# Kernel tuning notes

Hardware: AMD Instinct MI355X
Metric: run time of the kernel (lower is better)

The kernel has to match this reference:

```python
import jax, jax.numpy as jnp
import numpy as np
from jax import lax

PADDING = 1  # from init_kwargs; must equal (k-1)//2 so the residual add is shape-valid


def _conv_single(x, w):
    # x: [C_in, H, W], w: [C_out, C_in, kH, kW] -> [C_out, H, W]
    y = lax.conv_general_dilated(
        x[None],  # [1, C_in, H, W]
        w,
        window_strides=(1, 1),
        padding=[(PADDING, PADDING), (PADDING, PADDING)],
        dimension_numbers=("NCHW", "OIHW", "NCHW"),
    )
    return y[0]


def setup_inputs() -> dict:
    key = jax.random.key(0)
    k1, k2 = jax.random.split(key)
    B, C, H, W, K = 16, 128, 64, 64, 3
    inp = jax.random.normal(k1, (B, C, H, W), dtype=jnp.float32)
    # per-sample dynamic weights, scaled so conv output is O(1)
    weight = jax.random.normal(k2, (B, C, C, K, K), dtype=jnp.float32) * (1.0 / np.sqrt(C * K * K))
    return {"input": inp, "weight": weight}


def reference(input, weight):
    # per-sample conv2d with a different kernel per batch element + residual add
    residual = jax.vmap(_conv_single)(input, weight)  # [B, C, H, W]
    return input + residual
```

## Files before the change

### kernel.cpp

```cpp
#include <hip/hip_runtime.h>
#include <hip/hip_bf16.h>


typedef _Float16 h8 __attribute__((ext_vector_type(8)));
typedef _Float16 h4 __attribute__((ext_vector_type(4)));
typedef float f32x16 __attribute__((ext_vector_type(16)));
typedef float f4 __attribute__((ext_vector_type(4)));

#define MFMA32 __builtin_amdgcn_mfma_f32_32x32x16_f16

__global__ __launch_bounds__(256) void w_prepass(const float* __restrict__ W,
                                                 _Float16* __restrict__ wp) {
    __shared__ float raw[8 * 1153];
    const int bid = blockIdx.x;
    const int b   = bid >> 4;
    const int co0 = (bid & 15) * 8;
    const int t   = threadIdx.x;

    const float* src = W + (size_t)(b * 128 + co0) * 1152;
#pragma unroll
    for (int i = 0; i < 9; ++i) {
        int idx  = (i * 256 + t) * 4;
        f4 v     = *(const f4*)(src + idx);
        int co_l = idx / 1152;
        int rem  = idx - co_l * 1152;
        *(f4*)&raw[co_l * 1153 + rem] = v;
    }
    __syncthreads();

#pragma unroll
    for (int i = 0; i < 9; ++i) {
        int c    = i * 256 + t;
        int jh   = c & 1;
        int co_l = (c >> 1) & 7;
        int oct  = (c >> 4) & 3;
        int r    = c >> 6;
        int kw   = r % 3;
        int r2   = r / 3;
        int kc   = r2 & 3;
        int kh   = r2 >> 2;
        int cib  = kc * 32 + oct * 8 + jh * 4;
        h4 v;
#pragma unroll
        for (int jj = 0; jj < 4; ++jj)
            v[jj] = (_Float16)raw[co_l * 1153 + (cib + jj) * 9 + kh * 3 + kw];
        size_t o = ((size_t)(b * 3 + kh) * 4 + kc) * 12288 +
                   (size_t)(kw * 4 + oct) * 1024 + (size_t)(co0 + co_l) * 8 + jh * 4;
        *(h4*)&wp[o] = v;
    }
}


__global__ __launch_bounds__(256, 2) void conv_main(const float* __restrict__ X,
                                                    const _Float16* __restrict__ wp,
                                                    float* __restrict__ out) {
    __shared__ _Float16 sX[2 * 4 * 66 * 8];
    __shared__ _Float16 sW[12 * 128 * 8];

    const int t    = threadIdx.x;
    const int lane = t & 63;
    const int l31  = lane & 31;
    const int lhi  = lane >> 5;
    const int wv   = t >> 6;
    const int wvM  = wv >> 1;
    const int wr   = wv & 1;

    const int bid   = blockIdx.x;
    const int batch = bid >> 5;
    const int h0    = (bid & 31) * 2;

    const int sy  = t >> 7;
    const int xq  = (t & 15) * 4;
    const int cio = (t >> 4) & 7;

    f32x16 acc[2][2];
#pragma unroll
    for (int mt = 0; mt < 2; ++mt)
#pragma unroll
        for (int nt = 0; nt < 2; ++nt)
#pragma unroll
            for (int r = 0; r < 16; ++r) acc[mt][nt][r] = 0.f;

    if (t < 16) {
        int y = t >> 3, oct = (t >> 1) & 3, xp = (t & 1) * 65;
        h8 z;
#pragma unroll
        for (int j = 0; j < 8; ++j) z[j] = (_Float16)0.f;
        *(h8*)&sX[((y * 4 + oct) * 66 + xp) * 8] = z;
    }

    f4 xrv[4];
    h8 wreg[6];

    auto load_stage = [&](int s) {
        const int kh = s >> 2, kc = s & 3;
        const int yy = h0 + sy + kh - 1;
        if (yy >= 0 && yy < 64) {
            const float* xp = X + ((size_t)(batch * 128 + kc * 32 + cio * 4) * 64 + yy) * 64 + xq;
#pragma unroll
            for (int j = 0; j < 4; ++j) xrv[j] = *(const f4*)(xp + (size_t)j * 4096);
        } else {
#pragma unroll
            for (int j = 0; j < 4; ++j) xrv[j] = (f4){0.f, 0.f, 0.f, 0.f};
        }
        const _Float16* wsrc = wp + ((size_t)(batch * 3 + kh) * 4 + kc) * 12288 + t * 8;
#pragma unroll
        for (int r = 0; r < 6; ++r) wreg[r] = *(const h8*)(wsrc + (size_t)r * 2048);
    };
    auto write_stage = [&]() {
#pragma unroll
        for (int k = 0; k < 4; ++k) {
            h4 v = {(_Float16)xrv[0][k], (_Float16)xrv[1][k],
                    (_Float16)xrv[2][k], (_Float16)xrv[3][k]};
            *(h4*)&sX[((sy * 4 + (cio >> 1)) * 66 + xq + 1 + k) * 8 + (cio & 1) * 4] = v;
        }
#pragma unroll
        for (int r = 0; r < 6; ++r) *(h8*)&sW[(r * 256 + t) * 8] = wreg[r];
    };

    load_stage(0);
    __syncthreads();
    write_stage();
    __syncthreads();

#pragma unroll 1
    for (int s = 0; s < 12; ++s) {
        if (s < 11) load_stage(s + 1);

#pragma unroll
        for (int ks = 0; ks < 6; ++ks) {
            const int kw = ks >> 1, kk = ks & 1;
            h8 af[2], bf[2];
#pragma unroll
            for (int mt = 0; mt < 2; ++mt)
                af[mt] = *(const h8*)&sW[((kw * 4 + kk * 2 + lhi) * 128 + wvM * 64 + mt * 32 + l31) * 8];
#pragma unroll
            for (int nt = 0; nt < 2; ++nt)
                bf[nt] = *(const h8*)&sX[((wr * 4 + kk * 2 + lhi) * 66 + nt * 32 + l31 + kw) * 8];
#pragma unroll
            for (int mt = 0; mt < 2; ++mt)
#pragma unroll
                for (int nt = 0; nt < 2; ++nt)
                    acc[mt][nt] = MFMA32(af[mt], bf[nt], acc[mt][nt], 0, 0, 0);
        }

        if (s < 11) {
            __syncthreads();
            write_stage();
            __syncthreads();
        }
    }

#pragma unroll
    for (int mt = 0; mt < 2; ++mt)
#pragma unroll
        for (int nt = 0; nt < 2; ++nt)
#pragma unroll
            for (int rg = 0; rg < 16; ++rg) {
                int co = wvM * 64 + mt * 32 + (rg & 3) + 8 * (rg >> 2) + 4 * lhi;
                int x  = nt * 32 + l31;
                size_t o = ((size_t)(batch * 128 + co) * 64 + h0 + wr) * 64 + x;
                out[o] = X[o] + acc[mt][nt][rg];
            }
}

extern "C" void kernel_launch(void* const* d_in, const int* in_sizes, int n_in,
                              void* d_out, int out_size, void* d_ws, size_t ws_size,
                              hipStream_t stream) {
    const float* inp = (const float*)d_in[0];
    const float* wgt = (const float*)d_in[1];
    float* out = (float*)d_out;
    _Float16* wpk = (_Float16*)d_ws;

    w_prepass<<<256, 256, 0, stream>>>(wgt, wpk);
    conv_main<<<512, 256, 0, stream>>>(inp, wpk, out);
}
```

Before: 113.5 us.

## Double-buffer LDS and load weights directly to LDS via global_load_lds

Converts the single-buffered stage loop into a double-buffered pipeline with one barrier per stage instead of two. Weight tiles go straight from global memory into LDS through the global_load_lds builtin, with no register staging. Block indices are also swizzled so consecutive blocks map to different batches. LDS use grows to about 66KB per block, which may cut occupancy below the two blocks per CU requested by launch bounds.

```diff
diff --git a/kernel.cpp b/kernel.cpp
--- a/kernel.cpp
+++ b/kernel.cpp
@@ -8,6 +8,15 @@
 typedef float f4 __attribute__((ext_vector_type(4)));
 
 #define MFMA32 __builtin_amdgcn_mfma_f32_32x32x16_f16
+
+__device__ __forceinline__ void lds_load16(const void* g, void* l) {
+#if __has_builtin(__builtin_amdgcn_global_load_lds)
+    __builtin_amdgcn_global_load_lds((__attribute__((address_space(1))) const void*)g,
+                                     (__attribute__((address_space(3))) void*)l, 16, 0, 0);
+#else
+    *(f4*)l = *(const f4*)g;
+#endif
+}
 
 __global__ __launch_bounds__(256) void w_prepass(const float* __restrict__ W,
                                                  _Float16* __restrict__ wp) {
@@ -54,8 +63,8 @@
 __global__ __launch_bounds__(256, 2) void conv_main(const float* __restrict__ X,
                                                     const _Float16* __restrict__ wp,
                                                     float* __restrict__ out) {
-    __shared__ _Float16 sX[2 * 4 * 66 * 8];
-    __shared__ _Float16 sW[12 * 128 * 8];
+    __shared__ _Float16 sX[2 * 4224];
+    __shared__ _Float16 sW[2 * 12288];
 
     const int t    = threadIdx.x;
     const int lane = t & 63;
@@ -66,8 +75,9 @@
     const int wr   = wv & 1;
 
     const int bid   = blockIdx.x;
-    const int batch = bid >> 5;
-    const int h0    = (bid & 31) * 2;
+    const int swz   = (bid & 7) * 64 + (bid >> 3);
+    const int batch = swz >> 5;
+    const int h0    = (swz & 31) * 2;
 
     const int sy  = t >> 7;
     const int xq  = (t & 15) * 4;
@@ -81,19 +91,21 @@
 #pragma unroll
             for (int r = 0; r < 16; ++r) acc[mt][nt][r] = 0.f;
 
-    if (t < 16) {
-        int y = t >> 3, oct = (t >> 1) & 3, xp = (t & 1) * 65;
-        h8 z;
-#pragma unroll
-        for (int j = 0; j < 8; ++j) z[j] = (_Float16)0.f;
-        *(h8*)&sX[((y * 4 + oct) * 66 + xp) * 8] = z;
+    if (t < 32) {
+        int pb = t >> 4, y = (t >> 3) & 1, oct = (t >> 1) & 3, side = t & 1;
+        h8 z = {};
+        *(h8*)&sX[pb * 4224 + ((y * 4 + oct) * 66 + side * 65) * 8] = z;
     }
 
     f4 xrv[4];
-    h8 wreg[6];
 
-    auto load_stage = [&](int s) {
+    auto issue_stage = [&](int s, int pb) {
         const int kh = s >> 2, kc = s & 3;
+        const _Float16* wsrc = wp + ((size_t)(batch * 3 + kh) * 4 + kc) * 12288 + (size_t)t * 8;
+        _Float16* wdst = sW + pb * 12288 + t * 8;
+#pragma unroll
+        for (int r = 0; r < 6; ++r)
+            lds_load16(wsrc + (size_t)r * 2048, wdst + r * 2048);
         const int yy = h0 + sy + kh - 1;
         if (yy >= 0 && yy < 64) {
             const float* xp = X + ((size_t)(batch * 128 + kc * 32 + cio * 4) * 64 + yy) * 64 + xq;
@@ -103,53 +115,54 @@
 #pragma unroll
             for (int j = 0; j < 4; ++j) xrv[j] = (f4){0.f, 0.f, 0.f, 0.f};
         }
-        const _Float16* wsrc = wp + ((size_t)(batch * 3 + kh) * 4 + kc) * 12288 + t * 8;
-#pragma unroll
-        for (int r = 0; r < 6; ++r) wreg[r] = *(const h8*)(wsrc + (size_t)r * 2048);
     };
-    auto write_stage = [&]() {
+
+    auto write_x = [&](int pb) {
 #pragma unroll
         for (int k = 0; k < 4; ++k) {
             h4 v = {(_Float16)xrv[0][k], (_Float16)xrv[1][k],
                     (_Float16)xrv[2][k], (_Float16)xrv[3][k]};
-            *(h4*)&sX[((sy * 4 + (cio >> 1)) * 66 + xq + 1 + k) * 8 + (cio & 1) * 4] = v;
+            *(h4*)&sX[pb * 4224 + ((sy * 4 + (cio >> 1)) * 66 + xq + 1 + k) * 8 + (cio & 1) * 4] = v;
         }
-#pragma unroll
-        for (int r = 0; r < 6; ++r) *(h8*)&sW[(r * 256 + t) * 8] = wreg[r];
     };
 
-    load_stage(0);
-    __syncthreads();
-    write_stage();
-    __syncthreads();
-
-#pragma unroll 1
-    for (int s = 0; s < 12; ++s) {
-        if (s < 11) load_stage(s + 1);
-
+    auto compute = [&](int pb) {
+        const _Float16* sWp = sW + pb * 12288;
+        const _Float16* sXp = sX + pb * 4224;
 #pragma unroll
         for (int ks = 0; ks < 6; ++ks) {
             const int kw = ks >> 1, kk = ks & 1;
             h8 af[2], bf[2];
 #pragma unroll
             for (int mt = 0; mt < 2; ++mt)
-                af[mt] = *(const h8*)&sW[((kw * 4 + kk * 2 + lhi) * 128 + wvM * 64 + mt * 32 + l31) * 8];
+                af[mt] = *(const h8*)&sWp[((kw * 4 + kk * 2 + lhi) * 128 + wvM * 64 + mt * 32 + l31) * 8];
 #pragma unroll
             for (int nt = 0; nt < 2; ++nt)
-                bf[nt] = *(const h8*)&sX[((wr * 4 + kk * 2 + lhi) * 66 + nt * 32 + l31 + kw) * 8];
+                bf[nt] = *(const h8*)&sXp[((wr * 4 + kk * 2 + lhi) * 66 + nt * 32 + l31 + kw) * 8];
 #pragma unroll
             for (int mt = 0; mt < 2; ++mt)
 #pragma unroll
                 for (int nt = 0; nt < 2; ++nt)
                     acc[mt][nt] = MFMA32(af[mt], bf[nt], acc[mt][nt], 0, 0, 0);
         }
+    };
 
-        if (s < 11) {
-            __syncthreads();
-            write_stage();
-            __syncthreads();
-        }
+    issue_stage(0, 0);
+    write_x(0);
+    asm volatile("s_waitcnt vmcnt(0)" ::: "memory");
+    __syncthreads();
+
+    int p = 0;
+#pragma unroll 1
+    for (int s = 0; s < 11; ++s) {
+        issue_stage(s + 1, p ^ 1);
+        compute(p);
+        write_x(p ^ 1);
+        asm volatile("s_waitcnt vmcnt(0)" ::: "memory");
+        __syncthreads();
+        p ^= 1;
     }
+    compute(p);
 
 #pragma unroll
     for (int mt = 0; mt < 2; ++mt)
```

Result: no change. 111.8 us (-1.5%).
